# Optimization experiments

Hardware: AMD Instinct MI355X
Metric: run time of the kernel (lower is better)

The kernel has to match this reference:

```python
import jax, jax.numpy as jnp
import numpy as np

N_NODES = 100_000
N_EDGES = 1_600_000
IN_DIM, HIDDEN, Z_DIM = 64, 128, 64


def _gcn_conv(x, src, dst, dinv, W, b, n):
    # PyG GCNConv: out_i = sum_j (d_i^-1/2 d_j^-1/2) (x_j @ W) + b, edges incl. self-loops
    xw = x @ W                                   # [N, out]
    norm = dinv[src] * dinv[dst]                 # [E+N]
    msg = xw[src] * norm[:, None]                # [E+N, out]
    return jax.ops.segment_sum(msg, dst, num_segments=n) + b


def _prep_graph(edge_index, n):
    loop = jnp.arange(n, dtype=edge_index.dtype)
    src = jnp.concatenate([edge_index[0], loop])
    dst = jnp.concatenate([edge_index[1], loop])
    deg = jax.ops.segment_sum(jnp.ones_like(dst, dtype=jnp.float32), dst, num_segments=n)
    dinv = jnp.where(deg > 0, jax.lax.rsqrt(jnp.maximum(deg, 1.0)), 0.0)
    return src, dst, dinv


def setup_inputs() -> dict:
    key = jax.random.key(0)
    ks = jax.random.split(key, 8)
    x = jax.random.normal(ks[0], (N_NODES, IN_DIM), dtype=jnp.float32)
    edge_index = jax.random.randint(ks[1], (2, N_EDGES), 0, N_NODES, dtype=jnp.int32)

    def glorot(k, fi, fo):
        s = (6.0 / (fi + fo)) ** 0.5
        return jax.random.uniform(k, (fi, fo), jnp.float32, -s, s)

    return {
        "x": x, "edge_index": edge_index,
        "W1": glorot(ks[2], IN_DIM, HIDDEN), "b1": jnp.zeros((HIDDEN,), jnp.float32),
        "W2": glorot(ks[3], HIDDEN, HIDDEN), "b2": jnp.zeros((HIDDEN,), jnp.float32),
        "Wmu": glorot(ks[4], HIDDEN, Z_DIM), "bmu": jnp.zeros((Z_DIM,), jnp.float32),
        "Wlv": glorot(ks[5], HIDDEN, Z_DIM), "blv": jnp.zeros((Z_DIM,), jnp.float32),
    }


def reference(x, edge_index, W1, b1, W2, b2, Wmu, bmu, Wlv, blv):
    n = x.shape[0]
    src, dst, dinv = _prep_graph(edge_index, n)
    h = jax.nn.relu(_gcn_conv(x, src, dst, dinv, W1, b1, n))
    h = jax.nn.relu(_gcn_conv(h, src, dst, dinv, W2, b2, n))
    # dropout p=0.0 (eval): identity
    mu = _gcn_conv(h, src, dst, dinv, Wmu, bmu, n)
    logvar = _gcn_conv(h, src, dst, dinv, Wlv, blv, n)
    return (mu, logvar)
```

## Files before the change

kernel.cpp:

```cpp
#include <hip/hip_runtime.h>
#include <hip/hip_fp16.h>
#include <cstddef>

#define N_NODES 100000
#define N_EDGES 1600000
#define E_TOT   (N_EDGES + N_NODES)
#define IN_DIM  64
#define HIDDEN  128
#define Z_DIM   64

#define BN 128
#define NB ((N_NODES + BN - 1) / BN)
#define NCH 256

using f16x8 = __attribute__((ext_vector_type(8))) _Float16;
using f32x4 = __attribute__((ext_vector_type(4))) float;


__global__ __launch_bounds__(256) void prep_k(const float* __restrict__ x, __half* __restrict__ x16,
                                              const float* __restrict__ W1, const float* __restrict__ W2,
                                              const float* __restrict__ Wmu, const float* __restrict__ Wlv,
                                              __half* __restrict__ W1t, __half* __restrict__ W2t,
                                              __half* __restrict__ Wht,
                                              const int* __restrict__ dst, int* __restrict__ histG,
                                              int e, int nPrep) {
    __shared__ int hist[NB];
    int blk = blockIdx.x;
    int t = threadIdx.x;
    if (blk >= nPrep) {
        int c = blk - nPrep;
        int ch = (e + NCH - 1) / NCH;
        int i0 = c * ch, i1 = i0 + ch; if (i1 > e) i1 = e;
        for (int b = t; b < NB; b += 256) hist[b] = 0;
        __syncthreads();
        for (int i = i0 + t; i < i1; i += 256)
            atomicAdd(&hist[dst[i] >> 7], 1);
        __syncthreads();
        for (int b = t; b < NB; b += 256) histG[c * NB + b] = hist[b];
        return;
    }
    int i = blk * 256 + t;
    const int CAST = N_NODES * IN_DIM / 8;
    if (i < CAST) {
        const float4* in4 = (const float4*)x;
        float4 a = in4[2 * i], b = in4[2 * i + 1];
        __half2 h0 = __floats2half2_rn(a.x, a.y);
        __half2 h1 = __floats2half2_rn(a.z, a.w);
        __half2 h2 = __floats2half2_rn(b.x, b.y);
        __half2 h3 = __floats2half2_rn(b.z, b.w);
        uint4 pk = make_uint4(*(unsigned*)&h0, *(unsigned*)&h1, *(unsigned*)&h2, *(unsigned*)&h3);
        ((uint4*)x16)[i] = pk;
        return;
    }
    int j = i - CAST;
    if (j < 128 * 64) {
        int col = j >> 6, k = j & 63;
        W1t[j] = __float2half(W1[k * 128 + col]);
        return;
    }
    int m = j - 128 * 64;
    if (m < 128 * 128) {
        int col = m >> 7, k = m & 127;
        W2t[m] = __float2half(W2[k * 128 + col]);
        return;
    }
    int h = m - 128 * 128;
    if (h < 128 * 128) {
        int col = h >> 7, k = h & 127;
        Wht[h] = __float2half(col < 64 ? Wmu[k * 64 + col] : Wlv[k * 64 + (col - 64)]);
    }
}


__global__ __launch_bounds__(256) void boffB_k(int* __restrict__ histG, int* __restrict__ btot) {
    int wv = (int)((blockIdx.x * 256 + threadIdx.x) >> 6);
    if (wv >= NB) return;
    int lane = threadIdx.x & 63;
    int v[4];
#pragma unroll
    for (int k = 0; k < 4; k++) v[k] = histG[(4 * lane + k) * NB + wv];
    int s = v[0] + v[1] + v[2] + v[3];
    int run = s;
#pragma unroll
    for (int off = 1; off < 64; off <<= 1) {
        int tt = __shfl_up(run, off);
        if (lane >= off) run += tt;
    }
    int p = run - s;
#pragma unroll
    for (int k = 0; k < 4; k++) {
        int tt = v[k];
        histG[(4 * lane + k) * NB + wv] = p;
        p += tt;
    }
    if (lane == 63) btot[wv] = p;
}

__global__ __launch_bounds__(1024) void bscan_k(const int* __restrict__ btot, int* __restrict__ ebase, int e) {
    __shared__ int s[1024];
    int t = threadIdx.x;
    int v = (t < NB) ? btot[t] : 0;
    s[t] = v;
    __syncthreads();
#pragma unroll
    for (int off = 1; off < 1024; off <<= 1) {
        int x = (t >= off) ? s[t - off] : 0;
        __syncthreads();
        s[t] += x;
        __syncthreads();
    }
    if (t < NB) ebase[t] = s[t] - v;
    if (t == 0) ebase[NB] = e;
}

__global__ __launch_bounds__(256) void binB_k(const int* __restrict__ src, const int* __restrict__ dst,
                                              const int* __restrict__ boffs, const int* __restrict__ ebase,
                                              int* __restrict__ binned, int e) {
    __shared__ int cur[NB];
    int c = blockIdx.x, t = threadIdx.x;
    int ch = (e + NCH - 1) / NCH;
    int i0 = c * ch, i1 = i0 + ch; if (i1 > e) i1 = e;
    for (int b = t; b < NB; b += 256) cur[b] = ebase[b] + boffs[c * NB + b];
    __syncthreads();
    for (int i = i0 + t; i < i1; i += 256) {
        int s = src[i], d = dst[i];
        int p = atomicAdd(&cur[d >> 7], 1);
        binned[p] = ((d & 127) << 17) | s;
    }
}

__global__ __launch_bounds__(256) void pdeg_k(const int* __restrict__ binned, const int* __restrict__ ebase,
                                              int* __restrict__ rowptr, float* __restrict__ dinv, int n) {
    __shared__ int hist[BN];
    __shared__ int sc[BN];
    int b = blockIdx.x, t = threadIdx.x;
    int n0 = b * BN;
    int nn = n - n0; if (nn > BN) nn = BN;
    if (t < BN) hist[t] = (t < nn) ? 1 : 0;
    __syncthreads();
    int e0 = ebase[b], e1 = ebase[b + 1];
    for (int i = e0 + t; i < e1; i += 256)
        atomicAdd(&hist[binned[i] >> 17], 1);
    __syncthreads();
    int v = (t < BN) ? hist[t] : 0;
    if (t < BN) sc[t] = v;
    __syncthreads();
#pragma unroll
    for (int off = 1; off < BN; off <<= 1) {
        int x = (t < BN && t >= off) ? sc[t - off] : 0;
        __syncthreads();
        if (t < BN) sc[t] += x;
        __syncthreads();
    }
    int base = e0 + n0;
    if (t < nn) {
        rowptr[n0 + t] = base + sc[t] - v;
        dinv[n0 + t] = rsqrtf((float)v);
    }
    if (b == gridDim.x - 1 && t == 0) rowptr[n] = E_TOT;
}

__global__ __launch_bounds__(256) void pfill_k(const int* __restrict__ binned, const int* __restrict__ ebase,
                                               const int* __restrict__ rowptr, const float* __restrict__ dinv,
                                               int2* __restrict__ em, int n) {
    __shared__ int cur[BN];
    __shared__ float sdv[BN];
    int b = blockIdx.x, t = threadIdx.x;
    int n0 = b * BN;
    int nn = n - n0; if (nn > BN) nn = BN;
    if (t < nn) {
        int rp = rowptr[n0 + t];
        float dv = dinv[n0 + t];
        sdv[t] = dv;
        em[rp] = make_int2(n0 + t, __float_as_int(dv * dv));
        cur[t] = rp + 1;
    }
    __syncthreads();
    int e0 = ebase[b], e1 = ebase[b + 1];
    for (int i = e0 + t; i < e1; i += 256) {
        int pk = binned[i];
        int ld = pk >> 17, s = pk & 0x1FFFF;
        int q = atomicAdd(&cur[ld], 1);
        em[q] = make_int2(s, __float_as_int(dinv[s] * sdv[ld]));
    }
}


template <int DIM, bool HEAD>
__global__ __launch_bounds__(256) void agg_k(const __half* __restrict__ H, const int* __restrict__ rowptr,
                                             const int2* __restrict__ em, __half* __restrict__ out,
                                             const float* __restrict__ bmu, const float* __restrict__ blv,
                                             float* __restrict__ mu, float* __restrict__ lv, int n) {
    int node = (int)((blockIdx.x * 256 + threadIdx.x) >> 6);
    if (node >= n) return;
    int lane = threadIdx.x & 63;
    int beg = rowptr[node], end = rowptr[node + 1];
    const uint4* H4 = (const uint4*)H;

    constexpr int RV   = DIM / 8;
    constexpr int SUBS = 64 / RV;
    constexpr int STEP = SUBS * 2;
    int sub = lane / RV;
    int fl  = lane % RV;

    float acc[8];
#pragma unroll
    for (int q = 0; q < 8; q++) acc[q] = 0.f;

    auto meta = [&](int j, int p, int& s, float& w) {
        int idx = j + SUBS * p + sub;
        int ci  = idx < end ? idx : beg;
        int2 e  = em[ci];
        s = e.x;
        w = idx < end ? __int_as_float(e.y) : 0.f;
    };
    auto rows = [&](int s0, int s1, uint4& r0, uint4& r1) {
        r0 = H4[(size_t)s0 * RV + fl];
        r1 = H4[(size_t)s1 * RV + fl];
    };
    auto fmas = [&](const uint4& r0, const uint4& r1, float ww0, float ww1) {
        const __half* h0 = (const __half*)&r0;
        const __half* h1 = (const __half*)&r1;
#pragma unroll
        for (int q = 0; q < 8; q++) acc[q] = fmaf(ww0, __half2float(h0[q]), acc[q]);
#pragma unroll
        for (int q = 0; q < 8; q++) acc[q] = fmaf(ww1, __half2float(h1[q]), acc[q]);
    };

    int G = (end - beg + STEP - 1) / STEP;

    int   sa0, sa1, sb0, sb1, sc0, sc1, sd0, sd1;
    float wa0, wa1, wb0, wb1, wc0, wc1, wd0, wd1;
    uint4 ra0, ra1, rb0, rb1, rc0, rc1, rd0, rd1;

    meta(beg,            0, sa0, wa0); meta(beg,            1, sa1, wa1);
    meta(beg + STEP,     0, sb0, wb0); meta(beg + STEP,     1, sb1, wb1);
    rows(sa0, sa1, ra0, ra1);
    rows(sb0, sb1, rb0, rb1);
    meta(beg + 2 * STEP, 0, sc0, wc0); meta(beg + 2 * STEP, 1, sc1, wc1);
    meta(beg + 3 * STEP, 0, sd0, wd0); meta(beg + 3 * STEP, 1, sd1, wd1);

    int g = 0;
    int jf = beg + 4 * STEP;
    while (true) {
        rows(sc0, sc1, rc0, rc1);
        fmas(ra0, ra1, wa0, wa1);
        if (++g >= G) break;
        meta(jf, 0, sa0, wa0); meta(jf, 1, sa1, wa1); jf += STEP;

        rows(sd0, sd1, rd0, rd1);
        fmas(rb0, rb1, wb0, wb1);
        if (++g >= G) break;
        meta(jf, 0, sb0, wb0); meta(jf, 1, sb1, wb1); jf += STEP;

        rows(sa0, sa1, ra0, ra1);
        fmas(rc0, rc1, wc0, wc1);
        if (++g >= G) break;
        meta(jf, 0, sc0, wc0); meta(jf, 1, sc1, wc1); jf += STEP;

        rows(sb0, sb1, rb0, rb1);
        fmas(rd0, rd1, wd0, wd1);
        if (++g >= G) break;
        meta(jf, 0, sd0, wd0); meta(jf, 1, sd1, wd1); jf += STEP;
    }

#pragma unroll
    for (int off = 32; off >= RV; off >>= 1) {
#pragma unroll
        for (int q = 0; q < 8; q++) acc[q] += __shfl_xor(acc[q], off);
    }
    if (sub == 0) {
        if constexpr (HEAD) {
            const float* bp = (fl < 8) ? (bmu + fl * 8) : (blv + (fl - 8) * 8);
#pragma unroll
            for (int q = 0; q < 8; q++) acc[q] += bp[q];
            float* op = (fl < 8) ? (mu + (size_t)node * 64 + fl * 8)
                                 : (lv + (size_t)node * 64 + (fl - 8) * 8);
            *(float4*)op = make_float4(acc[0], acc[1], acc[2], acc[3]);
            *(float4*)(op + 4) = make_float4(acc[4], acc[5], acc[6], acc[7]);
        } else {
            __half2 q0 = __floats2half2_rn(acc[0], acc[1]);
            __half2 q1 = __floats2half2_rn(acc[2], acc[3]);
            __half2 q2 = __floats2half2_rn(acc[4], acc[5]);
            __half2 q3 = __floats2half2_rn(acc[6], acc[7]);
            uint4 pk = make_uint4(*(unsigned*)&q0, *(unsigned*)&q1, *(unsigned*)&q2, *(unsigned*)&q3);
            *(uint4*)(out + (size_t)node * DIM + fl * 8) = pk;
        }
    }
}


template <int K, bool BR>
__global__ __launch_bounds__(256) void mgemm_k(const __half* __restrict__ A,
                                               const __half* __restrict__ Wt,
                                               const float* __restrict__ bias,
                                               __half* __restrict__ C, int n) {
    __shared__ __align__(16) __half Wl[128 * K];
    int t = threadIdx.x;

    constexpr int CHUNKS = 128 * K / 8;
    const uint4* Wg = (const uint4*)Wt;
    for (int i = t; i < CHUNKS; i += 256) {
        int g = i * 16;
        int col = g / (2 * K);
        uint4 v = Wg[i];
        *(uint4*)((char*)Wl + (g ^ ((col & 7) << 4))) = v;
    }
    __syncthreads();

    int lane = t & 63, w = t >> 6;
    int colb = lane & 15;
    int kq = (lane >> 4) * 8;
    int m0 = blockIdx.x * 64 + w * 16;
    int rowA = m0 + colb; if (rowA >= n) rowA = n - 1;
    const __half* Arow = A + (size_t)rowA * K + kq;

    f32x4 acc[8];
#pragma unroll
    for (int c = 0; c < 8; c++) acc[c] = (f32x4){0.f, 0.f, 0.f, 0.f};

    const char* wb = (const char*)Wl;
    int swz = (colb & 7) << 4;
    int off0 = colb * (2 * K) + kq * 2;

#pragma unroll
    for (int k0 = 0; k0 < K; k0 += 32) {
        f16x8 a = *(const f16x8*)(Arow + k0);
#pragma unroll
        for (int c = 0; c < 8; c++) {
            f16x8 b = *(const f16x8*)(wb + ((off0 + c * (32 * K) + k0 * 2) ^ swz));
            acc[c] = __builtin_amdgcn_mfma_f32_16x16x32_f16(a, b, acc[c], 0, 0, 0);
        }
    }

    int rbase = m0 + (lane >> 4) * 4;
#pragma unroll
    for (int c = 0; c < 8; c++) {
        int col = c * 16 + colb;
        float bv = BR ? bias[col] : 0.f;
#pragma unroll
        for (int r = 0; r < 4; r++) {
            int row = rbase + r;
            if (row < n) {
                float v = acc[c][r] + bv;
                if (BR) v = fmaxf(v, 0.f);
                C[(size_t)row * 128 + col] = __float2half(v);
            }
        }
    }
}


__global__ __launch_bounds__(256) void mgemm2_k(const __half* __restrict__ A,
                                                const __half* __restrict__ W2t,
                                                const __half* __restrict__ Whtt,
                                                const float* __restrict__ b2,
                                                __half* __restrict__ P, int n) {
    constexpr int K = 128;
    __shared__ __align__(16) __half W2l[128 * K];
    __shared__ __align__(16) __half Tl[4 * 16 * 128];
    int t = threadIdx.x;

    const uint4* Wg = (const uint4*)W2t;
    for (int i = t; i < 128 * K / 8; i += 256) {
        int g = i * 16;
        int col = g / (2 * K);
        uint4 v = Wg[i];
        *(uint4*)((char*)W2l + (g ^ ((col & 7) << 4))) = v;
    }
    __syncthreads();

    int lane = t & 63, w = t >> 6;
    int colb = lane & 15;
    int kq = (lane >> 4) * 8;
    int m0 = blockIdx.x * 64 + w * 16;
    int rowA = m0 + colb; if (rowA >= n) rowA = n - 1;
    const __half* Arow = A + (size_t)rowA * K + kq;

    f32x4 acc[8];
#pragma unroll
    for (int c = 0; c < 8; c++) acc[c] = (f32x4){0.f, 0.f, 0.f, 0.f};

    const char* wb = (const char*)W2l;
    int swz = (colb & 7) << 4;
    int off0 = colb * (2 * K) + kq * 2;

#pragma unroll
    for (int k0 = 0; k0 < K; k0 += 32) {
        f16x8 a = *(const f16x8*)(Arow + k0);
#pragma unroll
        for (int c = 0; c < 8; c++) {
            f16x8 b = *(const f16x8*)(wb + ((off0 + c * (32 * K) + k0 * 2) ^ swz));
            acc[c] = __builtin_amdgcn_mfma_f32_16x16x32_f16(a, b, acc[c], 0, 0, 0);
        }
    }

    char* tb = (char*)Tl + w * 4096;
#pragma unroll
    for (int c = 0; c < 8; c++) {
        int col = c * 16 + colb;
        float bv = b2[col];
#pragma unroll
        for (int r = 0; r < 4; r++) {
            int rl = (lane >> 4) * 4 + r;
            float v = fmaxf(acc[c][r] + bv, 0.f);
            *(__half*)(tb + ((rl * 256 + col * 2) ^ ((rl & 7) << 4))) = __float2half(v);
        }
    }
    __syncthreads();

    f32x4 acc2[8];
#pragma unroll
    for (int c = 0; c < 8; c++) acc2[c] = (f32x4){0.f, 0.f, 0.f, 0.f};
    int arow = lane & 15;
    int aswz = (arow & 7) << 4;
#pragma unroll
    for (int k0 = 0; k0 < K; k0 += 32) {
        f16x8 a2 = *(const f16x8*)(tb + ((arow * 256 + (kq + k0) * 2) ^ aswz));
#pragma unroll
        for (int c = 0; c < 8; c++) {
            f16x8 b2f = *(const f16x8*)(Whtt + (size_t)(c * 16 + colb) * K + kq + k0);
            acc2[c] = __builtin_amdgcn_mfma_f32_16x16x32_f16(a2, b2f, acc2[c], 0, 0, 0);
        }
    }

    int rbase = m0 + (lane >> 4) * 4;
#pragma unroll
    for (int c = 0; c < 8; c++) {
        int col = c * 16 + colb;
#pragma unroll
        for (int r = 0; r < 4; r++) {
            int row = rbase + r;
            if (row < n) P[(size_t)row * 128 + col] = __float2half(acc2[c][r]);
        }
    }
}


extern "C" void kernel_launch(void* const* d_in, const int* in_sizes, int n_in,
                              void* d_out, int out_size, void* d_ws, size_t ws_size,
                              hipStream_t stream) {
    const int N = N_NODES, E = N_EDGES, ETOT = E_TOT;

    const float* x    = (const float*)d_in[0];
    const int*   ei   = (const int*)d_in[1];
    const int*   srcA = ei;
    const int*   dstA = ei + E;
    const float* W1   = (const float*)d_in[2];
    const float* b1   = (const float*)d_in[3];
    const float* W2   = (const float*)d_in[4];
    const float* b2   = (const float*)d_in[5];
    const float* Wmu  = (const float*)d_in[6];
    const float* bmu  = (const float*)d_in[7];
    const float* Wlv  = (const float*)d_in[8];
    const float* blv  = (const float*)d_in[9];
    float* out = (float*)d_out;

    char* ws = (char*)d_ws;
    size_t o = 0;
    auto alloc = [&](size_t bytes) -> void* {
        o = (o + 255) & ~(size_t)255;
        void* p = ws + o;
        o += bytes;
        return p;
    };
    int*    histG  = (int*)alloc((size_t)NCH * NB * 4);
    int*    btot   = (int*)alloc((size_t)NB * 4);
    int*    ebase  = (int*)alloc((size_t)(NB + 1) * 4);
    int*    rowptr = (int*)alloc((size_t)(N + 1) * 4);
    float*  dinv   = (float*)alloc((size_t)N * 4);
    int2*   em     = (int2*)alloc((size_t)ETOT * 8);
    int*    binned = (int*)alloc((size_t)E * 4);
    __half* x16    = (__half*)alloc((size_t)N * IN_DIM * 2);
    __half* B1     = (__half*)alloc((size_t)N * HIDDEN * 2);
    __half* B2     = (__half*)alloc((size_t)N * HIDDEN * 2);
    __half* W1t    = (__half*)alloc(128 * 64 * 2);
    __half* W2t    = (__half*)alloc(128 * 128 * 2);
    __half* Wht    = (__half*)alloc(128 * 128 * 2);
    (void)ws_size;

    const int PREP_T = N * IN_DIM / 8 + 128 * 64 + 128 * 128 + 128 * 128;
    const int nPrep = (PREP_T + 255) / 256;
    const int gAgg = (N + 3) / 4;
    const int gMg  = (N + 63) / 64;
    const int gBoff = (NB * 64 + 255) / 256;

    prep_k<<<nPrep + NCH, 256, 0, stream>>>(x, x16, W1, W2, Wmu, Wlv, W1t, W2t, Wht,
                                            dstA, histG, E, nPrep);
    boffB_k<<<gBoff, 256, 0, stream>>>(histG, btot);
    bscan_k<<<1, 1024, 0, stream>>>(btot, ebase, E);
    binB_k<<<NCH, 256, 0, stream>>>(srcA, dstA, histG, ebase, binned, E);
    pdeg_k<<<NB, 256, 0, stream>>>(binned, ebase, rowptr, dinv, N);
    pfill_k<<<NB, 256, 0, stream>>>(binned, ebase, rowptr, dinv, em, N);

    agg_k<64, false><<<gAgg, 256, 0, stream>>>(x16, rowptr, em, B1, nullptr, nullptr, nullptr, nullptr, N);
    mgemm_k<64, true><<<gMg, 256, 0, stream>>>(B1, W1t, b1, B2, N);

    agg_k<128, false><<<gAgg, 256, 0, stream>>>(B2, rowptr, em, B1, nullptr, nullptr, nullptr, nullptr, N);
    mgemm2_k<<<gMg, 256, 0, stream>>>(B1, W2t, Wht, b2, B2, N);

    agg_k<128, true><<<gAgg, 256, 0, stream>>>(B2, rowptr, em, nullptr, bmu, blv,
                                               out, out + (size_t)N * Z_DIM, N);
}
```

Measured before the change: 362.7 us.

## Sort nodes into degree buckets and process aggregation in degree order

New measurement: 376.2 us. 1.04x slower.

```diff
diff --git a/kernel.cpp b/kernel.cpp
--- a/kernel.cpp
+++ b/kernel.cpp
@@ -130,19 +130,23 @@
 }
 
 __global__ __launch_bounds__(256) void pdeg_k(const int* __restrict__ binned, const int* __restrict__ ebase,
-                                              int* __restrict__ rowptr, float* __restrict__ dinv, int n) {
+                                              int* __restrict__ rowptr, float* __restrict__ dinv,
+                                              int* __restrict__ histD, int n) {
     __shared__ int hist[BN];
     __shared__ int sc[BN];
+    __shared__ int hd[8];
     int b = blockIdx.x, t = threadIdx.x;
     int n0 = b * BN;
     int nn = n - n0; if (nn > BN) nn = BN;
     if (t < BN) hist[t] = (t < nn) ? 1 : 0;
+    if (t < 8) hd[t] = 0;
     __syncthreads();
     int e0 = ebase[b], e1 = ebase[b + 1];
     for (int i = e0 + t; i < e1; i += 256)
         atomicAdd(&hist[binned[i] >> 17], 1);
     __syncthreads();
     int v = (t < BN) ? hist[t] : 0;
+    if (t < nn) atomicAdd(&hd[min(v >> 3, 7)], 1);
     if (t < BN) sc[t] = v;
     __syncthreads();
 #pragma unroll
@@ -157,25 +161,66 @@
         rowptr[n0 + t] = base + sc[t] - v;
         dinv[n0 + t] = rsqrtf((float)v);
     }
+    if (t < 8) histD[b * 8 + t] = hd[t];
     if (b == gridDim.x - 1 && t == 0) rowptr[n] = E_TOT;
+}
+
+__global__ __launch_bounds__(1024) void dscan_k(const int* __restrict__ histD, int* __restrict__ doffs) {
+    __shared__ int s[1024];
+    const int TOT = NB * 8;
+    int t = threadIdx.x;
+    int base = t * 7;
+    int loc[7];
+    int sum = 0;
+#pragma unroll
+    for (int i = 0; i < 7; i++) {
+        int idx = base + i;
+        int v = 0;
+        if (idx < TOT) { int k = idx / NB, b = idx - k * NB; v = histD[b * 8 + k]; }
+        loc[i] = sum; sum += v;
+    }
+    s[t] = sum;
+    __syncthreads();
+#pragma unroll
+    for (int off = 1; off < 1024; off <<= 1) {
+        int x = (t >= off) ? s[t - off] : 0;
+        __syncthreads();
+        s[t] += x;
+        __syncthreads();
+    }
+    int ex = s[t] - sum;
+#pragma unroll
+    for (int i = 0; i < 7; i++) {
+        int idx = base + i;
+        if (idx < TOT) { int k = idx / NB, b = idx - k * NB; doffs[b * 8 + k] = ex + loc[i]; }
+    }
 }
 
 __global__ __launch_bounds__(256) void pfill_k(const int* __restrict__ binned, const int* __restrict__ ebase,
                                                const int* __restrict__ rowptr, const float* __restrict__ dinv,
+                                               const int* __restrict__ doffs, int* __restrict__ perm,
                                                int2* __restrict__ em, int n) {
     __shared__ int cur[BN];
     __shared__ float sdv[BN];
+    __shared__ int dcur[8];
     int b = blockIdx.x, t = threadIdx.x;
     int n0 = b * BN;
     int nn = n - n0; if (nn > BN) nn = BN;
+    if (t < 8) dcur[t] = doffs[b * 8 + t];
+    int rp = 0, deg = 0;
     if (t < nn) {
-        int rp = rowptr[n0 + t];
+        rp = rowptr[n0 + t];
+        deg = rowptr[n0 + t + 1] - rp;
         float dv = dinv[n0 + t];
         sdv[t] = dv;
         em[rp] = make_int2(n0 + t, __float_as_int(dv * dv));
         cur[t] = rp + 1;
     }
     __syncthreads();
+    if (t < nn) {
+        int r = atomicAdd(&dcur[min(deg >> 3, 7)], 1);
+        perm[r] = n0 + t;
+    }
     int e0 = ebase[b], e1 = ebase[b + 1];
     for (int i = e0 + t; i < e1; i += 256) {
         int pk = binned[i];
@@ -188,11 +233,13 @@
 
 template <int DIM, bool HEAD>
 __global__ __launch_bounds__(256) void agg_k(const __half* __restrict__ H, const int* __restrict__ rowptr,
-                                             const int2* __restrict__ em, __half* __restrict__ out,
+                                             const int2* __restrict__ em, const int* __restrict__ perm,
+                                             __half* __restrict__ out,
                                              const float* __restrict__ bmu, const float* __restrict__ blv,
                                              float* __restrict__ mu, float* __restrict__ lv, int n) {
-    int node = (int)((blockIdx.x * 256 + threadIdx.x) >> 6);
-    if (node >= n) return;
+    int wid = (int)((blockIdx.x * 256 + threadIdx.x) >> 6);
+    if (wid >= n) return;
+    int node = perm[wid];
     int lane = threadIdx.x & 63;
     int beg = rowptr[node], end = rowptr[node + 1];
     const uint4* H4 = (const uint4*)H;
@@ -469,6 +516,9 @@
     int*    ebase  = (int*)alloc((size_t)(NB + 1) * 4);
     int*    rowptr = (int*)alloc((size_t)(N + 1) * 4);
     float*  dinv   = (float*)alloc((size_t)N * 4);
+    int*    histD  = (int*)alloc((size_t)NB * 8 * 4);
+    int*    doffs  = (int*)alloc((size_t)NB * 8 * 4);
+    int*    perm   = (int*)alloc((size_t)N * 4);
     int2*   em     = (int2*)alloc((size_t)ETOT * 8);
     int*    binned = (int*)alloc((size_t)E * 4);
     __half* x16    = (__half*)alloc((size_t)N * IN_DIM * 2);
@@ -490,15 +540,18 @@
     boffB_k<<<gBoff, 256, 0, stream>>>(histG, btot);
     bscan_k<<<1, 1024, 0, stream>>>(btot, ebase, E);
     binB_k<<<NCH, 256, 0, stream>>>(srcA, dstA, histG, ebase, binned, E);
-    pdeg_k<<<NB, 256, 0, stream>>>(binned, ebase, rowptr, dinv, N);
-    pfill_k<<<NB, 256, 0, stream>>>(binned, ebase, rowptr, dinv, em, N);
-
-    agg_k<64, false><<<gAgg, 256, 0, stream>>>(x16, rowptr, em, B1, nullptr, nullptr, nullptr, nullptr, N);
+    pdeg_k<<<NB, 256, 0, stream>>>(binned, ebase, rowptr, dinv, histD, N);
+    dscan_k<<<1, 1024, 0, stream>>>(histD, doffs);
+    pfill_k<<<NB, 256, 0, stream>>>(binned, ebase, rowptr, dinv, doffs, perm, em, N);
+
+    agg_k<64, false><<<gAgg, 256, 0, stream>>>(x16, rowptr, em, perm, B1,
+                                               nullptr, nullptr, nullptr, nullptr, N);
     mgemm_k<64, true><<<gMg, 256, 0, stream>>>(B1, W1t, b1, B2, N);
 
-    agg_k<128, false><<<gAgg, 256, 0, stream>>>(B2, rowptr, em, B1, nullptr, nullptr, nullptr, nullptr, N);
+    agg_k<128, false><<<gAgg, 256, 0, stream>>>(B2, rowptr, em, perm, B1,
+                                                nullptr, nullptr, nullptr, nullptr, N);
     mgemm2_k<<<gMg, 256, 0, stream>>>(B1, W2t, Wht, b2, B2, N);
 
-    agg_k<128, true><<<gAgg, 256, 0, stream>>>(B2, rowptr, em, nullptr, bmu, blv,
+    agg_k<128, true><<<gAgg, 256, 0, stream>>>(B2, rowptr, em, perm, nullptr, bmu, blv,
                                                out, out + (size_t)N * Z_DIM, N);
 }
```
